# Performance work log

Measured on AMD Instinct MI355X. Metric: run time of the kernel, lower is better.

## Reference

```python
import jax, jax.numpy as jnp
import numpy as np
import math

DIM = 512
B, T, H, W = 1, 8, 64, 64


def setup_inputs() -> dict:
    key = jax.random.key(0)
    k0, k1, k2 = jax.random.split(key, 3)
    x = jax.random.normal(k0, (B, DIM, T, H, W), dtype=jnp.float32)
    gamma = jnp.ones((DIM,), jnp.float32)                      # RMS_norm gamma (viewed as flat vector)
    w_qkv = jax.random.normal(k1, (3 * DIM, DIM), jnp.float32) * 0.02  # conv1x1 weight (out, in)
    b_qkv = jnp.zeros((3 * DIM,), jnp.float32)
    w_proj = jax.random.normal(k2, (DIM, DIM), jnp.float32) * 0.02     # zero-init in torch; random for a meaningful baseline
    b_proj = jnp.zeros((DIM,), jnp.float32)
    return dict(x=x, gamma=gamma, w_qkv=w_qkv, b_qkv=b_qkv, w_proj=w_proj, b_proj=b_proj)


def reference(x, gamma, w_qkv, b_qkv, w_proj, b_proj):
    b, c, t, h, w = x.shape
    xt = jnp.transpose(x, (0, 2, 3, 4, 1))          # [b, t, h, w, c]
    identity = xt
    y = xt.reshape(b * t, h, w, c)
    # RMS_norm: L2 norm over channels (last dim), clamped, scaled by sqrt(c)*gamma
    norm = jnp.clip(jnp.linalg.norm(y, axis=-1, keepdims=True), 1e-12, None)
    y = y / norm * (c ** 0.5) * gamma
    # 1x1 conv QKV as GEMM over channels
    qkv = jnp.einsum('bhwc,oc->bhwo', y, w_qkv) + b_qkv        # [bt, h, w, 3c]
    qkv = qkv.reshape(b * t, h * w, 1, 3 * c)                  # nh=1 per source rearrange
    q, k, v = jnp.split(qkv, 3, axis=-1)                       # each [bt, hw, 1, c]
    scale = 1.0 / math.sqrt(c)
    # NOTE: hw sits in the batch position (faithful to source); seq len = nh = 1
    attn = jnp.einsum('bsnc,bsmc->bsnm', q, k) * scale         # [bt, hw, 1, 1]
    attn = jax.nn.softmax(attn, axis=-1)                       # trivially 1.0
    o = jnp.einsum('bsnm,bsmc->bsnc', attn, v)                 # == v
    o = o.reshape(b * t, h, w, c)
    o = jnp.einsum('bhwc,oc->bhwo', o, w_proj) + b_proj        # 1x1 proj conv
    o = o.reshape(b, t, h, w, c)
    out = jnp.transpose(o + identity, (0, 4, 1, 2, 3))         # back to [b, c, t, h, w]
    return out
```

## Files before the change

### kernel.cpp

```cpp
#include <hip/hip_runtime.h>

typedef unsigned short ushort_t;
typedef __attribute__((ext_vector_type(8))) short short8;
typedef __attribute__((ext_vector_type(4))) float f32x4;

#define DIMC 512
#define PN   32768
#define SQRTC 22.627416997969522f

__device__ __forceinline__ ushort_t f2bf(float f) {
  unsigned int u = __float_as_uint(f);
  unsigned int r = u + 0x7fffu + ((u >> 16) & 1u);
  return (ushort_t)(r >> 16);
}

__global__ __launch_bounds__(256) void k_cast(const float* __restrict__ a,
                                              ushort_t* __restrict__ b) {
  int i = (blockIdx.x * 256 + threadIdx.x) * 4;
  float4 v = *(const float4*)(a + i);
  ushort_t o[4] = {f2bf(v.x), f2bf(v.y), f2bf(v.z), f2bf(v.w)};
  *(uint2*)(b + i) = *(const uint2*)o;
}

__global__ __launch_bounds__(64) void k_wvt(const float* __restrict__ wqkv,
                                            ushort_t* __restrict__ WvT) {
  int c = blockIdx.x;
  int k8 = threadIdx.x * 8;
  ushort_t tmp[8];
#pragma unroll
  for (int j = 0; j < 8; ++j)
    tmp[j] = f2bf(wqkv[(long)(1024 + k8 + j) * DIMC + c]);
  *(uint4*)(WvT + (long)c * DIMC + k8) = *(const uint4*)tmp;
}

__global__ __launch_bounds__(256) void k_fb(const float* __restrict__ wp,
                                            const float* __restrict__ bqkv,
                                            const float* __restrict__ bproj,
                                            float* __restrict__ fb) {
  int wave = threadIdx.x >> 6;
  int lane = threadIdx.x & 63;
  int o = blockIdx.x * 4 + wave;
  float part = 0.f;
#pragma unroll
  for (int i = 0; i < 8; ++i) {
    int k = lane + i * 64;
    part += wp[o * DIMC + k] * bqkv[1024 + k];
  }
  for (int off = 32; off; off >>= 1) part += __shfl_down(part, off, 64);
  if (lane == 0) fb[o] = part + bproj[o];
}

__global__ __launch_bounds__(256) void k_gemm_w(
    const ushort_t* __restrict__ A,
    const ushort_t* __restrict__ BT,
    ushort_t* __restrict__ C,
    const float* __restrict__ gamma) {
  __shared__ ushort_t As[128 * 64];
  __shared__ ushort_t Bs[128 * 64];
  int tid = threadIdx.x;
  int p0 = blockIdx.x * 128;
  int o0 = blockIdx.y * 128;
  int wave = tid >> 6, lane = tid & 63;
  int wo = (wave & 1) * 64, wp = (wave >> 1) * 64;
  int q = lane >> 4, ln = lane & 15;

  f32x4 zero = {0.f, 0.f, 0.f, 0.f};
  f32x4 acc[4][4];
#pragma unroll
  for (int i = 0; i < 4; ++i)
#pragma unroll
    for (int j = 0; j < 4; ++j) acc[i][j] = zero;

  int sr = tid >> 3;
  int sc = tid & 7;
  const ushort_t* Ag = A + (long)(o0 + sr) * DIMC + sc * 8;
  const ushort_t* Bg = BT + (long)(p0 + sr) * DIMC + sc * 8;

  for (int kc = 0; kc < DIMC; kc += 64) {
    __syncthreads();
#pragma unroll
    for (int it = 0; it < 4; ++it) {
      int r = sr + it * 32;
      uint4 va = *(const uint4*)(Ag + (long)it * 32 * DIMC + kc);
      uint4 vb = *(const uint4*)(Bg + (long)it * 32 * DIMC + kc);
      int sw = ((sc ^ (r & 7)) * 8);
      *(uint4*)(&As[r * 64 + sw]) = va;
      *(uint4*)(&Bs[r * 64 + sw]) = vb;
    }
    __syncthreads();
#pragma unroll
    for (int ks = 0; ks < 2; ++ks) {
      int cch = ks * 4 + q;
      short8 af[4], bf[4];
#pragma unroll
      for (int mi = 0; mi < 4; ++mi) {
        int row = wo + mi * 16 + ln;
        af[mi] = *(const short8*)(&As[row * 64 + ((cch ^ (row & 7)) * 8)]);
      }
#pragma unroll
      for (int ni = 0; ni < 4; ++ni) {
        int row = wp + ni * 16 + ln;
        bf[ni] = *(const short8*)(&Bs[row * 64 + ((cch ^ (row & 7)) * 8)]);
      }
#pragma unroll
      for (int mi = 0; mi < 4; ++mi)
#pragma unroll
        for (int ni = 0; ni < 4; ++ni)
          acc[mi][ni] = __builtin_amdgcn_mfma_f32_16x16x32_bf16(af[mi], bf[ni], acc[mi][ni], 0, 0, 0);
    }
  }

#pragma unroll
  for (int mi = 0; mi < 4; ++mi) {
    int obase = o0 + wo + mi * 16 + q * 4;
#pragma unroll
    for (int ni = 0; ni < 4; ++ni) {
      int p = p0 + wp + ni * 16 + ln;
      float g = gamma[p];
#pragma unroll
      for (int r = 0; r < 4; ++r)
        C[(long)(obase + r) * DIMC + p] = f2bf(acc[mi][ni][r] * g);
    }
  }
}

__global__ __launch_bounds__(512, 4) void k_fused(
    const float* __restrict__ x,
    const ushort_t* __restrict__ Mp,
    const float* __restrict__ fb,
    float* __restrict__ out) {
  __shared__ ushort_t xs[8 * 64 * 64];
  __shared__ float red[32 * 65];
  __shared__ float s_sh[64];
  int tid = threadIdx.x;
  long p0 = (long)blockIdx.x * 64;

  int pl4 = (tid & 15) * 4;
  int kq  = tid >> 4;
  float ss0 = 0.f, ss1 = 0.f, ss2 = 0.f, ss3 = 0.f;
#pragma unroll
  for (int sw = 0; sw < 4; ++sw) {
    int k4 = kq * 4 + sw * 128;
    const float* xp = x + (long)k4 * PN + p0 + pl4;
    float4 v0 = *(const float4*)(xp);
    float4 v1 = *(const float4*)(xp + PN);
    float4 v2 = *(const float4*)(xp + 2 * PN);
    float4 v3 = *(const float4*)(xp + 3 * PN);
    ss0 += v0.x * v0.x + v1.x * v1.x + v2.x * v2.x + v3.x * v3.x;
    ss1 += v0.y * v0.y + v1.y * v1.y + v2.y * v2.y + v3.y * v3.y;
    ss2 += v0.z * v0.z + v1.z * v1.z + v2.z * v2.z + v3.z * v3.z;
    ss3 += v0.w * v0.w + v1.w * v1.w + v2.w * v2.w + v3.w * v3.w;
    ushort_t t0[4] = {f2bf(v0.x), f2bf(v1.x), f2bf(v2.x), f2bf(v3.x)};
    ushort_t t1[4] = {f2bf(v0.y), f2bf(v1.y), f2bf(v2.y), f2bf(v3.y)};
    ushort_t t2[4] = {f2bf(v0.z), f2bf(v1.z), f2bf(v2.z), f2bf(v3.z)};
    ushort_t t3[4] = {f2bf(v0.w), f2bf(v1.w), f2bf(v2.w), f2bf(v3.w)};
    char* base = (char*)xs + (k4 >> 6) * 8192;
    int ch  = (k4 >> 3) & 7;
    int sub = (k4 & 7) * 2;
    *(uint2*)(base + (pl4 + 0) * 128 + ((ch ^ ((pl4 + 0) & 7)) * 16) + sub) = *(const uint2*)t0;
    *(uint2*)(base + (pl4 + 1) * 128 + ((ch ^ ((pl4 + 1) & 7)) * 16) + sub) = *(const uint2*)t1;
    *(uint2*)(base + (pl4 + 2) * 128 + ((ch ^ ((pl4 + 2) & 7)) * 16) + sub) = *(const uint2*)t2;
    *(uint2*)(base + (pl4 + 3) * 128 + ((ch ^ ((pl4 + 3) & 7)) * 16) + sub) = *(const uint2*)t3;
  }
  red[kq * 65 + pl4 + 0] = ss0;
  red[kq * 65 + pl4 + 1] = ss1;
  red[kq * 65 + pl4 + 2] = ss2;
  red[kq * 65 + pl4 + 3] = ss3;
  __syncthreads();
  if (tid < 64) {
    float t = 0.f;
#pragma unroll
    for (int g = 0; g < 32; ++g) t += red[g * 65 + tid];
    s_sh[tid] = SQRTC / fmaxf(sqrtf(t), 1e-12f);
  }
  __syncthreads();

  int wave = tid >> 6, lane = tid & 63;
  int q = lane >> 4, ln = lane & 15;
  int wo = wave * 64;
  f32x4 zero = {0.f, 0.f, 0.f, 0.f};
  f32x4 acc[4][4];
#pragma unroll
  for (int i = 0; i < 4; ++i)
#pragma unroll
    for (int j = 0; j < 4; ++j) acc[i][j] = zero;

  const ushort_t* Ap = Mp + (long)wo * DIMC;
#pragma unroll 2
  for (int kb = 0; kb < 8; ++kb) {
    const char* bbase = (const char*)xs + kb * 8192;
#pragma unroll
    for (int ks = 0; ks < 2; ++ks) {
      int cch = ks * 4 + q;
      int kk = kb * 64 + cch * 8;
      short8 af[4], bf[4];
#pragma unroll
      for (int mi = 0; mi < 4; ++mi)
        af[mi] = *(const short8*)(Ap + (long)(mi * 16 + ln) * DIMC + kk);
#pragma unroll
      for (int ni = 0; ni < 4; ++ni) {
        int row = ni * 16 + ln;
        bf[ni] = *(const short8*)(bbase + row * 128 + ((cch ^ (row & 7)) * 16));
      }
#pragma unroll
      for (int mi = 0; mi < 4; ++mi)
#pragma unroll
        for (int ni = 0; ni < 4; ++ni)
          acc[mi][ni] = __builtin_amdgcn_mfma_f32_16x16x32_bf16(af[mi], bf[ni], acc[mi][ni], 0, 0, 0);
    }
  }

#pragma unroll
  for (int mi = 0; mi < 4; ++mi) {
    int obase = wo + mi * 16 + q * 4;
#pragma unroll
    for (int ni = 0; ni < 4; ++ni) {
      int plocal = ni * 16 + ln;
      long p = p0 + plocal;
      float sv = s_sh[plocal];
#pragma unroll
      for (int r = 0; r < 4; ++r) {
        int o = obase + r;
        out[(long)o * PN + p] = x[(long)o * PN + p] + fb[o] + sv * acc[mi][ni][r];
      }
    }
  }
}

extern "C" void kernel_launch(void* const* d_in, const int* in_sizes, int n_in,
                              void* d_out, int out_size, void* d_ws, size_t ws_size,
                              hipStream_t stream) {
  const float* x     = (const float*)d_in[0];
  const float* gamma = (const float*)d_in[1];
  const float* wqkv  = (const float*)d_in[2];
  const float* bqkv  = (const float*)d_in[3];
  const float* wproj = (const float*)d_in[4];
  const float* bproj = (const float*)d_in[5];

  char* ws = (char*)d_ws;
  ushort_t* Mp  = (ushort_t*)(ws);
  ushort_t* wpb = (ushort_t*)(ws + 524288);
  ushort_t* WvT = (ushort_t*)(ws + 1048576);
  float*    fb  = (float*)(ws + 1572864);

  k_cast<<<dim3(256), dim3(256), 0, stream>>>(wproj, wpb);
  k_wvt<<<dim3(512), dim3(64), 0, stream>>>(wqkv, WvT);
  k_fb<<<dim3(128), dim3(256), 0, stream>>>(wproj, bqkv, bproj, fb);
  k_gemm_w<<<dim3(4, 4), dim3(256), 0, stream>>>(wpb, WvT, Mp, gamma);
  k_fused<<<dim3(512), dim3(512), 0, stream>>>(x, Mp, fb, (float*)d_out);
}
```

Baseline: 174.8 us.

## Merge prep kernels, store folded weight in fragment order, prefetch A fragments

Folds the three small weight-preparation kernels into one launch to save launch overhead. The folded weight GEMM now writes its output in MFMA-fragment order, so each lane in the fused kernel does contiguous 16-byte loads instead of row-strided loads. The fused kernel also issues the first k-block's A fragments before the x load/normalize phase, fully unrolls the k loop, and uses a new LDS XOR swizzle key. The cost is more registers from the prefetched fragments and full unrolling, which could lower occupancy.

New measurement: 163.6 us. -6.4%, faster.

```diff
diff --git a/kernel.cpp b/kernel.cpp
--- a/kernel.cpp
+++ b/kernel.cpp
@@ -14,40 +14,41 @@
   return (ushort_t)(r >> 16);
 }
 
-__global__ __launch_bounds__(256) void k_cast(const float* __restrict__ a,
-                                              ushort_t* __restrict__ b) {
-  int i = (blockIdx.x * 256 + threadIdx.x) * 4;
-  float4 v = *(const float4*)(a + i);
-  ushort_t o[4] = {f2bf(v.x), f2bf(v.y), f2bf(v.z), f2bf(v.w)};
-  *(uint2*)(b + i) = *(const uint2*)o;
-}
-
-__global__ __launch_bounds__(64) void k_wvt(const float* __restrict__ wqkv,
-                                            ushort_t* __restrict__ WvT) {
-  int c = blockIdx.x;
-  int k8 = threadIdx.x * 8;
-  ushort_t tmp[8];
-#pragma unroll
-  for (int j = 0; j < 8; ++j)
-    tmp[j] = f2bf(wqkv[(long)(1024 + k8 + j) * DIMC + c]);
-  *(uint4*)(WvT + (long)c * DIMC + k8) = *(const uint4*)tmp;
-}
-
-__global__ __launch_bounds__(256) void k_fb(const float* __restrict__ wp,
-                                            const float* __restrict__ bqkv,
-                                            const float* __restrict__ bproj,
-                                            float* __restrict__ fb) {
-  int wave = threadIdx.x >> 6;
-  int lane = threadIdx.x & 63;
-  int o = blockIdx.x * 4 + wave;
-  float part = 0.f;
-#pragma unroll
-  for (int i = 0; i < 8; ++i) {
-    int k = lane + i * 64;
-    part += wp[o * DIMC + k] * bqkv[1024 + k];
-  }
-  for (int off = 32; off; off >>= 1) part += __shfl_down(part, off, 64);
-  if (lane == 0) fb[o] = part + bproj[o];
+__device__ __forceinline__ int kkey(int r) { return (r & 7) ^ ((r >> 2) & 7); }
+
+__global__ __launch_bounds__(256) void k_prep(const float* __restrict__ wproj,
+                                              const float* __restrict__ wqkv,
+                                              const float* __restrict__ bqkv,
+                                              const float* __restrict__ bproj,
+                                              ushort_t* __restrict__ wpb,
+                                              ushort_t* __restrict__ WvT,
+                                              float* __restrict__ fb) {
+  int bid = blockIdx.x, tid = threadIdx.x;
+  if (bid < 256) {
+    int i = (bid * 256 + tid) * 4;
+    float4 v = *(const float4*)(wproj + i);
+    ushort_t o[4] = {f2bf(v.x), f2bf(v.y), f2bf(v.z), f2bf(v.w)};
+    *(uint2*)(wpb + i) = *(const uint2*)o;
+  } else if (bid < 384) {
+    int c = (bid - 256) * 4 + (tid >> 6);
+    int k8 = (tid & 63) * 8;
+    ushort_t tmp[8];
+#pragma unroll
+    for (int j = 0; j < 8; ++j)
+      tmp[j] = f2bf(wqkv[(long)(1024 + k8 + j) * DIMC + c]);
+    *(uint4*)(WvT + (long)c * DIMC + k8) = *(const uint4*)tmp;
+  } else {
+    int wave = tid >> 6, lane = tid & 63;
+    int o = (bid - 384) * 4 + wave;
+    float part = 0.f;
+#pragma unroll
+    for (int i = 0; i < 8; ++i) {
+      int k = lane + i * 64;
+      part += wproj[o * DIMC + k] * bqkv[1024 + k];
+    }
+    for (int off = 32; off; off >>= 1) part += __shfl_down(part, off, 64);
+    if (lane == 0) fb[o] = part + bproj[o];
+  }
 }
 
 __global__ __launch_bounds__(256) void k_gemm_w(
@@ -115,18 +116,23 @@
     int obase = o0 + wo + mi * 16 + q * 4;
 #pragma unroll
     for (int ni = 0; ni < 4; ++ni) {
-      int p = p0 + wp + ni * 16 + ln;
-      float g = gamma[p];
-#pragma unroll
-      for (int r = 0; r < 4; ++r)
-        C[(long)(obase + r) * DIMC + p] = f2bf(acc[mi][ni][r] * g);
+      int c = p0 + wp + ni * 16 + ln;
+      float g = gamma[c];
+      int kb2 = c >> 6, ks2 = (c >> 5) & 1, q2 = (c >> 3) & 3, j2 = c & 7;
+#pragma unroll
+      for (int r = 0; r < 4; ++r) {
+        int o = obase + r;
+        int w2 = o >> 6, mi2 = (o >> 4) & 3, ln2 = o & 15;
+        long idx = (((((long)w2 * 8 + kb2) * 2 + ks2) * 4 + mi2) * 64 + q2 * 16 + ln2) * 8 + j2;
+        C[idx] = f2bf(acc[mi][ni][r] * g);
+      }
     }
   }
 }
 
 __global__ __launch_bounds__(512, 4) void k_fused(
     const float* __restrict__ x,
-    const ushort_t* __restrict__ Mp,
+    const ushort_t* __restrict__ Mp2,
     const float* __restrict__ fb,
     float* __restrict__ out) {
   __shared__ ushort_t xs[8 * 64 * 64];
@@ -134,6 +140,14 @@
   __shared__ float s_sh[64];
   int tid = threadIdx.x;
   long p0 = (long)blockIdx.x * 64;
+
+  int wave = tid >> 6, lane = tid & 63;
+  int q = lane >> 4, ln = lane & 15;
+
+  const ushort_t* Aw = Mp2 + (long)wave * 32768 + lane * 8;
+  short8 a0[8];
+#pragma unroll
+  for (int f = 0; f < 8; ++f) a0[f] = *(const short8*)(Aw + f * 512);
 
   int pl4 = (tid & 15) * 4;
   int kq  = tid >> 4;
@@ -157,10 +171,10 @@
     char* base = (char*)xs + (k4 >> 6) * 8192;
     int ch  = (k4 >> 3) & 7;
     int sub = (k4 & 7) * 2;
-    *(uint2*)(base + (pl4 + 0) * 128 + ((ch ^ ((pl4 + 0) & 7)) * 16) + sub) = *(const uint2*)t0;
-    *(uint2*)(base + (pl4 + 1) * 128 + ((ch ^ ((pl4 + 1) & 7)) * 16) + sub) = *(const uint2*)t1;
-    *(uint2*)(base + (pl4 + 2) * 128 + ((ch ^ ((pl4 + 2) & 7)) * 16) + sub) = *(const uint2*)t2;
-    *(uint2*)(base + (pl4 + 3) * 128 + ((ch ^ ((pl4 + 3) & 7)) * 16) + sub) = *(const uint2*)t3;
+    *(uint2*)(base + (pl4 + 0) * 128 + ((ch ^ kkey(pl4 + 0)) * 16) + sub) = *(const uint2*)t0;
+    *(uint2*)(base + (pl4 + 1) * 128 + ((ch ^ kkey(pl4 + 1)) * 16) + sub) = *(const uint2*)t1;
+    *(uint2*)(base + (pl4 + 2) * 128 + ((ch ^ kkey(pl4 + 2)) * 16) + sub) = *(const uint2*)t2;
+    *(uint2*)(base + (pl4 + 3) * 128 + ((ch ^ kkey(pl4 + 3)) * 16) + sub) = *(const uint2*)t3;
   }
   red[kq * 65 + pl4 + 0] = ss0;
   red[kq * 65 + pl4 + 1] = ss1;
@@ -175,9 +189,6 @@
   }
   __syncthreads();
 
-  int wave = tid >> 6, lane = tid & 63;
-  int q = lane >> 4, ln = lane & 15;
-  int wo = wave * 64;
   f32x4 zero = {0.f, 0.f, 0.f, 0.f};
   f32x4 acc[4][4];
 #pragma unroll
@@ -185,22 +196,21 @@
 #pragma unroll
     for (int j = 0; j < 4; ++j) acc[i][j] = zero;
 
-  const ushort_t* Ap = Mp + (long)wo * DIMC;
-#pragma unroll 2
+#pragma unroll
   for (int kb = 0; kb < 8; ++kb) {
     const char* bbase = (const char*)xs + kb * 8192;
 #pragma unroll
     for (int ks = 0; ks < 2; ++ks) {
+      short8 af[4], bf[4];
+#pragma unroll
+      for (int mi = 0; mi < 4; ++mi)
+        af[mi] = (kb == 0) ? a0[ks * 4 + mi]
+                           : *(const short8*)(Aw + ((kb * 2 + ks) * 4 + mi) * 512);
       int cch = ks * 4 + q;
-      int kk = kb * 64 + cch * 8;
-      short8 af[4], bf[4];
-#pragma unroll
-      for (int mi = 0; mi < 4; ++mi)
-        af[mi] = *(const short8*)(Ap + (long)(mi * 16 + ln) * DIMC + kk);
 #pragma unroll
       for (int ni = 0; ni < 4; ++ni) {
         int row = ni * 16 + ln;
-        bf[ni] = *(const short8*)(bbase + row * 128 + ((cch ^ (row & 7)) * 16));
+        bf[ni] = *(const short8*)(bbase + row * 128 + ((cch ^ kkey(row)) * 16));
       }
 #pragma unroll
       for (int mi = 0; mi < 4; ++mi)
@@ -210,6 +220,7 @@
     }
   }
 
+  int wo = wave * 64;
 #pragma unroll
   for (int mi = 0; mi < 4; ++mi) {
     int obase = wo + mi * 16 + q * 4;
@@ -238,14 +249,12 @@
   const float* bproj = (const float*)d_in[5];
 
   char* ws = (char*)d_ws;
-  ushort_t* Mp  = (ushort_t*)(ws);
+  ushort_t* Mp2 = (ushort_t*)(ws);
   ushort_t* wpb = (ushort_t*)(ws + 524288);
   ushort_t* WvT = (ushort_t*)(ws + 1048576);
   float*    fb  = (float*)(ws + 1572864);
 
-  k_cast<<<dim3(256), dim3(256), 0, stream>>>(wproj, wpb);
-  k_wvt<<<dim3(512), dim3(64), 0, stream>>>(wqkv, WvT);
-  k_fb<<<dim3(128), dim3(256), 0, stream>>>(wproj, bqkv, bproj, fb);
-  k_gemm_w<<<dim3(4, 4), dim3(256), 0, stream>>>(wpb, WvT, Mp, gamma);
-  k_fused<<<dim3(512), dim3(512), 0, stream>>>(x, Mp, fb, (float*)d_out);
-}
+  k_prep<<<dim3(512), dim3(256), 0, stream>>>(wproj, wqkv, bqkv, bproj, wpb, WvT, fb);
+  k_gemm_w<<<dim3(4, 4), dim3(256), 0, stream>>>(wpb, WvT, Mp2, gamma);
+  k_fused<<<dim3(512), dim3(512), 0, stream>>>(x, Mp2, fb, (float*)d_out);
+}
```
